# Optimization experiments

Measured on AMD Instinct MI355X. Metric: run time of the kernel, lower is better.

## Reference

```python
import jax, jax.numpy as jnp
import numpy as np

HN, ND, STRIDE, ESTRIDE = 10, 40, 3, 3  # hidden_node, ndim, stride, encode_stride


def _build_graphs():
    # Dense aggregation matrices A[dst, src] equivalent to the module's fixed
    # edge lists (scatter-add of src features into dst). Graph is tiny (10/40
    # nodes) and identical across the batch, so dense matmul is the efficient
    # exact form of the gather->scatter-add.
    w = np.float32(np.exp(-(1.0 / STRIDE) ** 2))
    A_pred = np.zeros((HN, HN), np.float32)
    for j in range(HN):
        A_pred[j, j] += 1.0                      # edge [j, j], weight 1
        for dj in range(1, STRIDE - 1):          # dj = 1 only
            A_pred[(j - dj) % HN, j] += w        # edge [j, j-dj]
            A_pred[(j + dj) % HN, j] += w        # edge [j, j+dj]
    A_enc = np.zeros((HN, ND), np.float32)
    A_dec = np.zeros((ND, HN), np.float32)
    for j in range(HN):
        cg = (j * ND // HN) % ND                 # center_grid = 4j
        for i in range(cg - ESTRIDE, cg + ESTRIDE):
            A_enc[j, i % ND] += 1.0              # grid i -> hidden j
            A_dec[i % ND, j] += 1.0              # hidden j -> grid i
    return jnp.asarray(A_enc), jnp.asarray(A_pred), jnp.asarray(A_dec)

A_ENC, A_PRED, A_DEC = _build_graphs()


def setup_inputs() -> dict:
    key = jax.random.key(0)
    ks = jax.random.split(key, 12)
    B, HF = 524288, 8
    s = 0.3  # modest weight scale
    return {
        "x": jax.random.normal(ks[0], (B, ND), jnp.float32),
        "z": jax.random.uniform(ks[1], (B, HN, HF), dtype=jnp.float32),
        "y": jax.random.uniform(ks[2], (B, ND, 1), dtype=jnp.float32),
        "enc_rel_w": jax.random.normal(ks[3], (HF, 1), jnp.float32) * s,
        "enc_rel_b": jax.random.normal(ks[4], (HF,), jnp.float32) * s,
        "enc_root_w": jax.random.normal(ks[5], (HF, HF), jnp.float32) * s,
        "pred_rel_w": jax.random.normal(ks[6], (HF, HF), jnp.float32) * s,
        "pred_rel_b": jax.random.normal(ks[7], (HF,), jnp.float32) * s,
        "pred_root_w": jax.random.normal(ks[8], (HF, HF), jnp.float32) * s,
        "dec_rel_w": jax.random.normal(ks[9], (1, HF), jnp.float32) * s,
        "dec_rel_b": jax.random.normal(ks[10], (1,), jnp.float32) * s,
        "dec_root_w": jax.random.normal(ks[11], (1, 1), jnp.float32) * s,
    }


def reference(x, z, y, enc_rel_w, enc_rel_b, enc_root_w,
              pred_rel_w, pred_rel_b, pred_root_w,
              dec_rel_w, dec_rel_b, dec_root_w):
    xb = x[..., None]  # [B, 40, 1]
    # encoder GraphConv((1, 8) -> 8): lin_rel(agg(x_src)) + lin_root(z)
    agg = jnp.einsum('ds,bsf->bdf', A_ENC, xb)                 # [B, 10, 1]
    z1 = jax.nn.relu(agg @ enc_rel_w.T + enc_rel_b + z @ enc_root_w.T)
    # predictor GraphConv(8 -> 8) with edge weights folded into A_PRED
    agg2 = jnp.einsum('ds,bsf->bdf', A_PRED, z1)               # [B, 10, 8]
    z2 = jax.nn.relu(agg2 @ pred_rel_w.T + pred_rel_b + z1 @ pred_root_w.T)
    # decoder GraphConv((8, 1) -> 1)
    agg3 = jnp.einsum('ds,bsf->bdf', A_DEC, z2)                # [B, 40, 8]
    out = agg3 @ dec_rel_w.T + dec_rel_b + y @ dec_root_w.T   # [B, 40, 1]
    return out[..., 0]                                         # [B, 40]
```

## Files before the change

kernel.cpp:

```cpp
#include <hip/hip_runtime.h>


#define HN 10
#define ND 40
#define HF 8
#define TPB 256

__global__ __launch_bounds__(TPB) void gnn_kernel(
    const float* __restrict__ x,
    const float* __restrict__ z,
    const float* __restrict__ y,
    const float* __restrict__ enc_rel_w,
    const float* __restrict__ enc_rel_b,
    const float* __restrict__ enc_root_w,
    const float* __restrict__ pred_rel_w,
    const float* __restrict__ pred_rel_b,
    const float* __restrict__ pred_root_w,
    const float* __restrict__ dec_rel_w,
    const float* __restrict__ dec_rel_b,
    const float* __restrict__ dec_root_w,
    float* __restrict__ out,
    int B)
{
    const long long e = (long long)blockIdx.x * TPB + threadIdx.x;

    const float w = 0.8948393168143698f;

    const float4* xr = (const float4*)(x + e * ND);
    float xv[ND];
    #pragma unroll
    for (int k = 0; k < 10; ++k) {
        float4 v = xr[k];
        xv[4*k+0] = v.x; xv[4*k+1] = v.y; xv[4*k+2] = v.z; xv[4*k+3] = v.w;
    }

    float agg[HN];
    agg[0] = xv[37] + xv[38] + xv[39] + xv[0] + xv[1] + xv[2];
    #pragma unroll
    for (int j = 1; j < HN; ++j)
        agg[j] = xv[4*j-3] + xv[4*j-2] + xv[4*j-1] + xv[4*j] + xv[4*j+1] + xv[4*j+2];

    const float4* zr = (const float4*)(z + e * (HN * HF));

    auto enc_row = [&](float4 v0, float4 v1, int j, float (&r)[HF]) {
        float zrow[HF] = {v0.x, v0.y, v0.z, v0.w, v1.x, v1.y, v1.z, v1.w};
        #pragma unroll
        for (int f = 0; f < HF; ++f) {
            float acc = agg[j] * enc_rel_w[f] + enc_rel_b[f];
            #pragma unroll
            for (int g = 0; g < HF; ++g)
                acc += zrow[g] * enc_root_w[f * HF + g];
            r[f] = fmaxf(acc, 0.0f);
        }
    };

    auto emit = [&](const float (&rm)[HF], const float (&rc)[HF],
                    const float (&rp)[HF]) -> float {
        float a2[HF];
        #pragma unroll
        for (int f = 0; f < HF; ++f)
            a2[f] = rc[f] + w * (rm[f] + rp[f]);
        float s = 0.0f;
        #pragma unroll
        for (int f = 0; f < HF; ++f) {
            float acc = pred_rel_b[f];
            #pragma unroll
            for (int g = 0; g < HF; ++g)
                acc += a2[g] * pred_rel_w[f * HF + g];
            #pragma unroll
            for (int g = 0; g < HF; ++g)
                acc += rc[g] * pred_root_w[f * HF + g];
            s += fmaxf(acc, 0.0f) * dec_rel_w[f];
        }
        return s;
    };

    float rA[5][HF], rB[5][HF];
    {
        float4 zA[10];
        #pragma unroll
        for (int k = 0; k < 10; ++k) zA[k] = zr[k];
        #pragma unroll
        for (int jj = 0; jj < 5; ++jj) enc_row(zA[2*jj], zA[2*jj+1], jj, rA[jj]);
    }
    {
        float4 zB[10];
        #pragma unroll
        for (int k = 0; k < 10; ++k) zB[k] = zr[10 + k];
        #pragma unroll
        for (int jj = 0; jj < 5; ++jj) enc_row(zB[2*jj], zB[2*jj+1], 5 + jj, rB[jj]);
    }

    const float4* yr = (const float4*)(y + e * ND);
    float4 yv[10];
    #pragma unroll
    for (int k = 0; k < 10; ++k) yv[k] = yr[k];

    float s2[HN];
    s2[1] = emit(rA[0], rA[1], rA[2]);
    s2[2] = emit(rA[1], rA[2], rA[3]);
    s2[3] = emit(rA[2], rA[3], rA[4]);
    s2[4] = emit(rA[3], rA[4], rB[0]);
    s2[5] = emit(rA[4], rB[0], rB[1]);
    s2[6] = emit(rB[0], rB[1], rB[2]);
    s2[7] = emit(rB[1], rB[2], rB[3]);
    s2[8] = emit(rB[2], rB[3], rB[4]);
    s2[9] = emit(rB[3], rB[4], rA[0]);
    s2[0] = emit(rB[4], rA[0], rA[1]);

    const float drb   = dec_rel_b[0];
    const float droot = dec_root_w[0];
    float4* og = (float4*)(out + e * ND);
    #pragma unroll
    for (int k = 0; k < 10; ++k) {
        const int k1 = (k + 1) % HN;
        const float pair = s2[k] + s2[k1] + drb;
        float4 o;
        o.x = (s2[k]  + drb) + yv[k].x * droot;
        o.y = pair           + yv[k].y * droot;
        o.z = pair           + yv[k].z * droot;
        o.w = (s2[k1] + drb) + yv[k].w * droot;
        og[k] = o;
    }
}

extern "C" void kernel_launch(void* const* d_in, const int* in_sizes, int n_in,
                              void* d_out, int out_size, void* d_ws, size_t ws_size,
                              hipStream_t stream) {
    const float* x          = (const float*)d_in[0];
    const float* z          = (const float*)d_in[1];
    const float* y          = (const float*)d_in[2];
    const float* enc_rel_w  = (const float*)d_in[3];
    const float* enc_rel_b  = (const float*)d_in[4];
    const float* enc_root_w = (const float*)d_in[5];
    const float* pred_rel_w = (const float*)d_in[6];
    const float* pred_rel_b = (const float*)d_in[7];
    const float* pred_root_w= (const float*)d_in[8];
    const float* dec_rel_w  = (const float*)d_in[9];
    const float* dec_rel_b  = (const float*)d_in[10];
    const float* dec_root_w = (const float*)d_in[11];
    float* out = (float*)d_out;

    const int B = in_sizes[0] / ND;
    const int blocks = B / TPB;
    gnn_kernel<<<blocks, TPB, 0, stream>>>(
        x, z, y, enc_rel_w, enc_rel_b, enc_root_w,
        pred_rel_w, pred_rel_b, pred_root_w,
        dec_rel_w, dec_rel_b, dec_root_w, out, B);
}
```

Measured before the change: 420.1 us.

## Stream hidden nodes through rolling window with software-prefetched loads

Replaces the fully unrolled load-everything-then-compute structure with a rolling loop over hidden nodes. Each iteration keeps a three-row window of encoder outputs, prefetches the next x/z chunk and the current y chunk, and writes output as it goes. This cuts the number of live registers (roughly 80 z floats, 40 x, 40 y and 80 encoder outputs before) to raise occupancy and overlap memory with compute. The catch is a non-unrolled loop with dynamic indexing and fewer loads in flight per thread.

```diff
diff --git a/kernel.cpp b/kernel.cpp
--- a/kernel.cpp
+++ b/kernel.cpp
@@ -27,26 +27,18 @@
     const float w = 0.8948393168143698f;
 
     const float4* xr = (const float4*)(x + e * ND);
-    float xv[ND];
-    #pragma unroll
-    for (int k = 0; k < 10; ++k) {
-        float4 v = xr[k];
-        xv[4*k+0] = v.x; xv[4*k+1] = v.y; xv[4*k+2] = v.z; xv[4*k+3] = v.w;
-    }
+    const float4* zr = (const float4*)(z + e * (HN * HF));
+    const float4* yr = (const float4*)(y + e * ND);
+    float4*       og = (float4*)(out + e * ND);
 
-    float agg[HN];
-    agg[0] = xv[37] + xv[38] + xv[39] + xv[0] + xv[1] + xv[2];
-    #pragma unroll
-    for (int j = 1; j < HN; ++j)
-        agg[j] = xv[4*j-3] + xv[4*j-2] + xv[4*j-1] + xv[4*j] + xv[4*j+1] + xv[4*j+2];
+    const float drb   = dec_rel_b[0];
+    const float droot = dec_root_w[0];
 
-    const float4* zr = (const float4*)(z + e * (HN * HF));
-
-    auto enc_row = [&](float4 v0, float4 v1, int j, float (&r)[HF]) {
+    auto enc_row = [&](float aggv, float4 v0, float4 v1, float (&r)[HF]) {
         float zrow[HF] = {v0.x, v0.y, v0.z, v0.w, v1.x, v1.y, v1.z, v1.w};
         #pragma unroll
         for (int f = 0; f < HF; ++f) {
-            float acc = agg[j] * enc_rel_w[f] + enc_rel_b[f];
+            float acc = aggv * enc_rel_w[f] + enc_rel_b[f];
             #pragma unroll
             for (int g = 0; g < HF; ++g)
                 acc += zrow[g] * enc_root_w[f * HF + g];
@@ -75,53 +67,65 @@
         return s;
     };
 
-    float rA[5][HF], rB[5][HF];
-    {
-        float4 zA[10];
+    auto store_out = [&](int idx, float sa, float sb, float4 yv) {
+        const float pair = sa + sb + drb;
+        float4 o;
+        o.x = (sa + drb) + yv.x * droot;
+        o.y = pair       + yv.y * droot;
+        o.z = pair       + yv.z * droot;
+        o.w = (sb + drb) + yv.w * droot;
+        og[idx] = o;
+    };
+
+    float4 X9 = xr[9];
+    float4 Xa = xr[0];
+    float4 Xb = xr[1];
+    float4 Xc = xr[2];
+    float4 z00 = zr[0], z01 = zr[1];
+    float4 z10 = zr[2], z11 = zr[3];
+    float4 zc0 = zr[4], zc1 = zr[5];
+
+    const float agg0 = X9.y + X9.z + X9.w + Xa.x + Xa.y + Xa.z;
+    const float agg1 = Xa.y + Xa.z + Xa.w + Xb.x + Xb.y + Xb.z;
+    float aggn       = Xb.y + Xb.z + Xb.w + Xc.x + Xc.y + Xc.z;
+
+    float r0s[HF], r1s[HF];
+    enc_row(agg0, z00, z01, r0s);
+    enc_row(agg1, z10, z11, r1s);
+
+    float rm[HF], rc[HF];
+    #pragma unroll
+    for (int f = 0; f < HF; ++f) { rm[f] = r0s[f]; rc[f] = r1s[f]; }
+
+    float s2p = 0.0f, s2_1 = 0.0f;
+
+    #pragma unroll 1
+    for (int k = 1; k <= 8; ++k) {
+        int kn = k + 2; if (kn > 9) kn -= 10;
+        float4 Xn  = xr[kn];
+        float4 zn0 = zr[2 * kn];
+        float4 zn1 = zr[2 * kn + 1];
+        float4 yv  = yr[k - 1];
+
+        float rp[HF];
+        enc_row(aggn, zc0, zc1, rp);
+        float s2c = emit(rm, rc, rp);
+
+        if (k == 1) s2_1 = s2c;
+        if (k >= 2) store_out(k - 1, s2p, s2c, yv);
+
+        aggn = Xc.y + Xc.z + Xc.w + Xn.x + Xn.y + Xn.z;
+        Xc = Xn; zc0 = zn0; zc1 = zn1;
         #pragma unroll
-        for (int k = 0; k < 10; ++k) zA[k] = zr[k];
-        #pragma unroll
-        for (int jj = 0; jj < 5; ++jj) enc_row(zA[2*jj], zA[2*jj+1], jj, rA[jj]);
-    }
-    {
-        float4 zB[10];
-        #pragma unroll
-        for (int k = 0; k < 10; ++k) zB[k] = zr[10 + k];
-        #pragma unroll
-        for (int jj = 0; jj < 5; ++jj) enc_row(zB[2*jj], zB[2*jj+1], 5 + jj, rB[jj]);
+        for (int f = 0; f < HF; ++f) { rm[f] = rc[f]; rc[f] = rp[f]; }
+        s2p = s2c;
     }
 
-    const float4* yr = (const float4*)(y + e * ND);
-    float4 yv[10];
-    #pragma unroll
-    for (int k = 0; k < 10; ++k) yv[k] = yr[k];
-
-    float s2[HN];
-    s2[1] = emit(rA[0], rA[1], rA[2]);
-    s2[2] = emit(rA[1], rA[2], rA[3]);
-    s2[3] = emit(rA[2], rA[3], rA[4]);
-    s2[4] = emit(rA[3], rA[4], rB[0]);
-    s2[5] = emit(rA[4], rB[0], rB[1]);
-    s2[6] = emit(rB[0], rB[1], rB[2]);
-    s2[7] = emit(rB[1], rB[2], rB[3]);
-    s2[8] = emit(rB[2], rB[3], rB[4]);
-    s2[9] = emit(rB[3], rB[4], rA[0]);
-    s2[0] = emit(rB[4], rA[0], rA[1]);
-
-    const float drb   = dec_rel_b[0];
-    const float droot = dec_root_w[0];
-    float4* og = (float4*)(out + e * ND);
-    #pragma unroll
-    for (int k = 0; k < 10; ++k) {
-        const int k1 = (k + 1) % HN;
-        const float pair = s2[k] + s2[k1] + drb;
-        float4 o;
-        o.x = (s2[k]  + drb) + yv[k].x * droot;
-        o.y = pair           + yv[k].y * droot;
-        o.z = pair           + yv[k].z * droot;
-        o.w = (s2[k1] + drb) + yv[k].w * droot;
-        og[k] = o;
-    }
+    const float s2_9 = emit(rm, rc, r0s);
+    store_out(8, s2p, s2_9, yr[8]);
+    const float s2_0 = emit(rc, r0s, r1s);
+    store_out(9, s2_9, s2_0, yr[9]);
+    store_out(0, s2_0, s2_1, yr[0]);
 }
 
 extern "C" void kernel_launch(void* const* d_in, const int* in_sizes, int n_in,
```

After: 567.6 us. +35.1%, slower.
